# Kernel tuning notes

Hardware: AMD Instinct MI355X
Metric: run time of the kernel (lower is better)

## Reference

```python
import jax, jax.numpy as jnp
import numpy as np

B, N, D, L = 16, 100, 1024, 2000


def setup_inputs() -> dict:
    key = jax.random.key(0)
    ks = jax.random.split(key, 9)
    s = 1.0 / np.sqrt(D)
    return {
        "feature": jax.random.normal(ks[0], (B, N, D), dtype=jnp.float32),
        "graph": jax.random.randint(ks[1], (B, N, N), 0, L),
        "W0": jax.random.normal(ks[2], (D, D), dtype=jnp.float32) * s,
        "W1": jax.random.normal(ks[3], (D, D), dtype=jnp.float32) * s,
        "bias": jax.random.uniform(ks[4], (L, D), dtype=jnp.float32, minval=-s, maxval=s),
        "dp_Wa": jax.random.normal(ks[5], (D, D), dtype=jnp.float32) * s,
        "dp_ba": jax.random.normal(ks[6], (D,), dtype=jnp.float32) * s,
        "dp_Wb": jax.random.normal(ks[7], (D, D), dtype=jnp.float32) * s,
        "dp_bb": jax.random.normal(ks[8], (D,), dtype=jnp.float32) * s,
        "get_alpha": 0,
    }


def reference(feature, graph, W0, W1, bias, dp_Wa, dp_ba, dp_Wb, dp_bb, get_alpha):
    # ---- DirectedGraphConv.conv ----
    adj = (graph != 0).astype(feature.dtype)                     # [B,N,N]
    out = feature + feature @ W0.T + feature @ W1.T              # [B,N,D]
    out = out + jnp.take(bias, graph, axis=0).sum(axis=2)        # label-embedding gather+sum over neighbors
    # ---- relation_alpha: DotProduct(feature, feature) ----
    a = feature @ dp_Wa.T + dp_ba                                # [B,N,D]
    b = feature @ dp_Wb.T + dp_bb                                # [B,N,D]
    alpha = jnp.einsum('bik,bjk->bij', a, b)                     # [B,N,N]
    alpha = jnp.maximum(alpha, 0.0)                              # alpha[alpha<0]=0
    alpha = jnp.einsum('bij,bjk->bik', adj, alpha)               # bmm(adj, alpha)
    alpha = jax.nn.softmax(alpha, axis=1)                        # Softmax(dim=1)
    out = jnp.einsum('bij,bjk->bik', alpha, out)                 # bmm(alpha, output)
    if get_alpha:
        return (out, alpha)
    return out
```

## Files before the change

kernel.cpp:

```cpp
#include <hip/hip_runtime.h>
#include <stdint.h>

#define B_   16
#define N_   100
#define D_   1024
#define L_   2000
#define M_   1600

#define ZCAP 64
#define RCAP 24
#define TC   12

typedef __bf16 bf16x8 __attribute__((ext_vector_type(8)));
typedef float  f32x4  __attribute__((ext_vector_type(4)));

__device__ __forceinline__ void gl_lds16(const __bf16* g, __bf16* l) {
    __builtin_amdgcn_global_load_lds(
        (const __attribute__((address_space(1))) void*)g,
        (__attribute__((address_space(3))) void*)l, 16, 0, 0);
}


__global__ void __launch_bounds__(256)
k_prep(const float* __restrict__ f,
       const float* __restrict__ W0, const float* __restrict__ W1,
       const float* __restrict__ Wa, const float* __restrict__ Wb,
       const float* __restrict__ bias,
       __bf16* __restrict__ fb, __bf16* __restrict__ wcat, __bf16* __restrict__ biasB) {
    int i = blockIdx.x * 256 + threadIdx.x;
    union { __bf16 h[8]; uint4 u; } pk;
    if (i < 204800) {
        long base = (long)i * 8;
        const float4* p = (const float4*)(f + base);
        float4 x = p[0], y = p[1];
        pk.h[0]=(__bf16)x.x; pk.h[1]=(__bf16)x.y; pk.h[2]=(__bf16)x.z; pk.h[3]=(__bf16)x.w;
        pk.h[4]=(__bf16)y.x; pk.h[5]=(__bf16)y.y; pk.h[6]=(__bf16)y.z; pk.h[7]=(__bf16)y.w;
        ((uint4*)fb)[i] = pk.u;
    } else if (i < 598016) {
        int j = i - 204800;
        long base = (long)j * 8;
        long seg = base >> 20;
        long off = base & ((1l << 20) - 1);
        if (seg == 0) {
            const float4* p0 = (const float4*)(W0 + off);
            const float4* p1 = (const float4*)(W1 + off);
            float4 a0 = p0[0], a1 = p0[1], b0 = p1[0], b1 = p1[1];
            pk.h[0]=(__bf16)(a0.x+b0.x); pk.h[1]=(__bf16)(a0.y+b0.y);
            pk.h[2]=(__bf16)(a0.z+b0.z); pk.h[3]=(__bf16)(a0.w+b0.w);
            pk.h[4]=(__bf16)(a1.x+b1.x); pk.h[5]=(__bf16)(a1.y+b1.y);
            pk.h[6]=(__bf16)(a1.z+b1.z); pk.h[7]=(__bf16)(a1.w+b1.w);
        } else {
            const float* src = (seg == 1) ? Wa : Wb;
            const float4* p = (const float4*)(src + off);
            float4 x = p[0], y = p[1];
            pk.h[0]=(__bf16)x.x; pk.h[1]=(__bf16)x.y; pk.h[2]=(__bf16)x.z; pk.h[3]=(__bf16)x.w;
            pk.h[4]=(__bf16)y.x; pk.h[5]=(__bf16)y.y; pk.h[6]=(__bf16)y.z; pk.h[7]=(__bf16)y.w;
        }
        ((uint4*)wcat)[j] = pk.u;
    } else {
        int j = i - 598016;
        long base = (long)j * 8;
        const float4* p = (const float4*)(bias + base);
        float4 x = p[0], y = p[1];
        pk.h[0]=(__bf16)x.x; pk.h[1]=(__bf16)x.y; pk.h[2]=(__bf16)x.z; pk.h[3]=(__bf16)x.w;
        pk.h[4]=(__bf16)y.x; pk.h[5]=(__bf16)y.y; pk.h[6]=(__bf16)y.z; pk.h[7]=(__bf16)y.w;
        ((uint4*)biasB)[j] = pk.u;
    }
}


#define BM 64
#define BN 128
#define BK 64

__global__ void __launch_bounds__(256)
k_gemm(const __bf16* __restrict__ A, const __bf16* __restrict__ Bw,
       const float* __restrict__ feat, const float* __restrict__ ba,
       const float* __restrict__ bbias,
       float* __restrict__ out0, float* __restrict__ aB, float* __restrict__ bB) {
    __shared__ __align__(16) __bf16 As[BM * BK];
    __shared__ __align__(16) __bf16 Bs[BN * BK];
    int t = threadIdx.x;
    int bm = blockIdx.x, bn = blockIdx.y;
    int lane = t & 63, wave = t >> 6;
    int wr = wave & 1, wc = wave >> 1;
    int lrow = lane & 15, quad = lane >> 4;

    f32x4 acc[2][4] = {};
    const __bf16* Ag = A  + (long)(bm * BM) * D_;
    const __bf16* Bg = Bw + (long)(bn * BN) * D_;

    for (int k0 = 0; k0 < D_; k0 += BK) {
        #pragma unroll
        for (int pi = 0; pi < 2; ++pi) {
            int p = pi * 256 + t, row = p >> 3, c = (p & 7) ^ (row & 7);
            gl_lds16(Ag + (long)row * D_ + k0 + c * 8, As + p * 8);
        }
        #pragma unroll
        for (int pi = 0; pi < 4; ++pi) {
            int p = pi * 256 + t, row = p >> 3, c = (p & 7) ^ (row & 7);
            gl_lds16(Bg + (long)row * D_ + k0 + c * 8, Bs + p * 8);
        }
        __syncthreads();
        #pragma unroll
        for (int ks = 0; ks < 2; ++ks) {
            bf16x8 af[2], bf[4];
            #pragma unroll
            for (int i = 0; i < 2; ++i) {
                int r = wr * 32 + i * 16 + lrow;
                int slot = r * 8 + (((ks << 2) | quad) ^ (r & 7));
                af[i] = *(const bf16x8*)(As + slot * 8);
            }
            #pragma unroll
            for (int j = 0; j < 4; ++j) {
                int r = wc * 64 + j * 16 + lrow;
                int slot = r * 8 + (((ks << 2) | quad) ^ (r & 7));
                bf[j] = *(const bf16x8*)(Bs + slot * 8);
            }
            #pragma unroll
            for (int i = 0; i < 2; ++i)
                #pragma unroll
                for (int j = 0; j < 4; ++j)
                    acc[i][j] = __builtin_amdgcn_mfma_f32_16x16x32_bf16(af[i], bf[j], acc[i][j], 0, 0, 0);
        }
        __syncthreads();
    }

    int nbase = bn * BN;
    int seg = nbase >> 10;
    #pragma unroll
    for (int i = 0; i < 2; ++i) {
        int gm0 = bm * BM + wr * 32 + i * 16 + quad * 4;
        #pragma unroll
        for (int j = 0; j < 4; ++j) {
            int col = (nbase + wc * 64 + j * 16 + lrow) & 1023;
            #pragma unroll
            for (int r = 0; r < 4; ++r) {
                long m = gm0 + r;
                float v = acc[i][j][r];
                if (seg == 0)      out0[m * D_ + col] = v + feat[m * D_ + col];
                else if (seg == 1) aB[m * D_ + col]   = v + ba[col];
                else               bB[m * D_ + col]   = v + bbias[col];
            }
        }
    }
}


__global__ void __launch_bounds__(256)
k_gather(const int* __restrict__ graph, const __bf16* __restrict__ biasB,
         float* __restrict__ out0) {
    int bi = blockIdx.x;
    int t = threadIdx.x;
    __shared__ int idxs[N_];
    if (t < N_) idxs[t] = graph[(long)bi * N_ + t];
    __syncthreads();
    float a0 = 0.f, a1 = 0.f, a2 = 0.f, a3 = 0.f;
    for (int j = 0; j < N_; ++j) {
        int lb = idxs[j];
        union { uint2 u; __bf16 h[4]; } pk;
        pk.u = ((const uint2*)(biasB + (long)lb * D_))[t];
        a0 += (float)pk.h[0]; a1 += (float)pk.h[1];
        a2 += (float)pk.h[2]; a3 += (float)pk.h[3];
    }
    float4* o = (float4*)(out0 + (long)bi * D_) + t;
    float4 cur = *o;
    cur.x += a0; cur.y += a1; cur.z += a2; cur.w += a3;
    *o = cur;
}


__global__ void __launch_bounds__(256)
k_scan(const int* __restrict__ graph, int* __restrict__ meta) {
    int b = blockIdx.x, t = threadIdx.x;
    __shared__ int cnt, ndvS;
    __shared__ int zi[ZCAP], zj[ZCAP], pr[ZCAP], di[RCAP];
    if (t == 0) cnt = 0;
    __syncthreads();
    const int* g = graph + (long)b * N_ * N_;
    for (int p = t; p < N_ * N_; p += 256) {
        if (g[p] == 0) {
            int pos = atomicAdd(&cnt, 1);
            if (pos < ZCAP) { zi[pos] = p / N_; zj[pos] = p % N_; }
        }
    }
    __syncthreads();
    if (t == 0) {
        int Z = min(cnt, ZCAP), n = 0;
        for (int q = 0; q < Z; ++q) {
            int r = -1;
            for (int s = 0; s < n; ++s) if (di[s] == zi[q]) { r = s; break; }
            if (r < 0 && n < RCAP) { di[n] = zi[q]; r = n; ++n; }
            pr[q] = r;
        }
        ndvS = n;
    }
    __syncthreads();
    int Z = min(cnt, ZCAP), n = ndvS;
    int* mb = meta + b * 256;
    if (t == 0) { mb[0] = Z; mb[1] = n; }
    if (t < Z) { mb[2 + t] = zj[t]; mb[66 + t] = pr[t]; }
    if (t < n) mb[130 + t] = di[t];
    if (t < N_) {
        int m = 0;
        for (int r = 0; r < n; ++r) if (di[r] == t) m = 1 + r;
        mb[154 + t] = m;
    }
}


__global__ void __launch_bounds__(256)
k_alpha(const int* __restrict__ meta, const float* __restrict__ aB,
        const float* __restrict__ bB, float* __restrict__ wl, float* __restrict__ cwG) {
    int b = blockIdx.x, kc = blockIdx.y;
    int t = threadIdx.x, lane = t & 63, wave = t >> 6;
    const int* mb = meta + b * 256;
    int Z = mb[0], ndv = mb[1];
    __shared__ int zjL[ZCAP], prL[ZCAP];
    __shared__ float corrL[RCAP][4];
    __shared__ float wred[4][4];
    if (t < Z) { zjL[t] = mb[2 + t]; prL[t] = mb[66 + t]; }
    if (t < RCAP * 4) corrL[t >> 2][t & 3] = 0.f;
    __syncthreads();

    int k0 = kc * 4;
    float4 bv[4];
    #pragma unroll
    for (int kk = 0; kk < 4; ++kk)
        bv[kk] = *(const float4*)(bB + ((long)(b * N_ + k0 + kk)) * D_ + t * 4);

    for (int q = 0; q < Z; ++q) {
        const float* ar = aB + ((long)(b * N_ + zjL[q])) * D_;
        float4 av = *(const float4*)(ar + t * 4);
        float s[4];
        #pragma unroll
        for (int kk = 0; kk < 4; ++kk)
            s[kk] = av.x * bv[kk].x + av.y * bv[kk].y + av.z * bv[kk].z + av.w * bv[kk].w;
        #pragma unroll
        for (int off = 32; off > 0; off >>= 1)
            #pragma unroll
            for (int kk = 0; kk < 4; ++kk) s[kk] += __shfl_xor(s[kk], off);
        if (lane == 0) { wred[wave][0]=s[0]; wred[wave][1]=s[1]; wred[wave][2]=s[2]; wred[wave][3]=s[3]; }
        __syncthreads();
        if (t < 4) {
            float v = wred[0][t] + wred[1][t] + wred[2][t] + wred[3][t];
            v = fmaxf(v, 0.f);
            int r = prL[q];
            if (r >= 0) corrL[r][t] += v;
        }
        __syncthreads();
    }

    if (t < 4) {
        int k = k0 + t;
        float denom = (float)(N_ - ndv);
        for (int r = 0; r < ndv; ++r) {
            float e = __expf(-corrL[r][t]);
            corrL[r][t] = e;
            denom += e;
        }
        float w = 1.f / denom;
        wl[b * N_ + k] = w;
        for (int r = 0; r < ndv; ++r)
            cwG[((long)b * RCAP + r) * N_ + k] = corrL[r][t] * w;
    }
}


__global__ void __launch_bounds__(256)
k_mix(const int* __restrict__ meta, const float* __restrict__ wl,
      const float* __restrict__ cwG, const float* __restrict__ out0,
      float* __restrict__ out) {
    int b = blockIdx.x, dq = blockIdx.y;
    int t = threadIdx.x, c = t & 127, h = t >> 7;
    int d0 = dq * 128;
    const int* mb = meta + b * 256;
    int ndv = mb[1], ntask = ndv + 1;
    __shared__ float wT[TC][N_];
    __shared__ float parts[2][TC][128];
    __shared__ int mapL[N_];
    if (t < N_) mapL[t] = mb[154 + t];

    const float* o0 = out0 + (long)b * N_ * D_ + d0;
    for (int cb = 0; cb < ntask; cb += TC) {
        for (int idx = t; idx < TC * N_; idx += 256) {
            int rr = idx / N_, j = idx - rr * N_;
            int task = cb + rr;
            float v = 0.f;
            if (task == 0)         v = wl[b * N_ + j];
            else if (task <= ndv)  v = cwG[((long)b * RCAP + task - 1) * N_ + j];
            wT[rr][j] = v;
        }
        __syncthreads();
        float acc[TC] = {};
        #pragma unroll 2
        for (int j = h * 50; j < h * 50 + 50; ++j) {
            float v = o0[(long)j * D_ + c];
            #pragma unroll
            for (int rr = 0; rr < TC; ++rr) acc[rr] += wT[rr][j] * v;
        }
        #pragma unroll
        for (int rr = 0; rr < TC; ++rr) parts[h][rr][c] = acc[rr];
        __syncthreads();
        for (int i = h * 50; i < h * 50 + 50; ++i) {
            int task = mapL[i];
            if (task >= cb && task < cb + TC) {
                int rr = task - cb;
                out[((long)(b * N_ + i)) * D_ + d0 + c] = parts[0][rr][c] + parts[1][rr][c];
            }
        }
        __syncthreads();
    }
}


extern "C" void kernel_launch(void* const* d_in, const int* in_sizes, int n_in,
                              void* d_out, int out_size, void* d_ws, size_t ws_size,
                              hipStream_t stream) {
    const float* feature = (const float*)d_in[0];
    const int*   graph   = (const int*)d_in[1];
    const float* W0      = (const float*)d_in[2];
    const float* W1      = (const float*)d_in[3];
    const float* bias    = (const float*)d_in[4];
    const float* dp_Wa   = (const float*)d_in[5];
    const float* dp_ba   = (const float*)d_in[6];
    const float* dp_Wb   = (const float*)d_in[7];
    const float* dp_bb   = (const float*)d_in[8];
    float* out = (float*)d_out;

    char* w = (char*)d_ws;
    __bf16* fb16  = (__bf16*)(w);
    __bf16* wcat  = (__bf16*)(w + 3276800);
    __bf16* biasB = (__bf16*)(w + 9568256);
    float*  out0  = (float*)(w + 13664256);
    float*  aB    = (float*)(w + 20217856);
    float*  bB    = (float*)(w + 26771456);
    int*    meta  = (int*)(w + 33325056);
    float*  wl    = (float*)(w + 33341440);
    float*  cwG   = (float*)(w + 33347840);

    k_prep<<<3336, 256, 0, stream>>>(feature, W0, W1, dp_Wa, dp_Wb, bias,
                                     fb16, wcat, biasB);
    k_gemm<<<dim3(25, 24), 256, 0, stream>>>(fb16, wcat, feature, dp_ba, dp_bb,
                                             out0, aB, bB);
    k_gather<<<1600, 256, 0, stream>>>(graph, biasB, out0);
    k_scan<<<B_, 256, 0, stream>>>(graph, meta);
    k_alpha<<<dim3(B_, 25), 256, 0, stream>>>(meta, aB, bB, wl, cwG);
    k_mix<<<dim3(B_, 8), 256, 0, stream>>>(meta, wl, cwG, out0, out);
}
```

Measured before the change: 179.3 us.

## Double-buffer LDS tiles in projection GEMM to overlap loads with MFMA

```diff
diff --git a/kernel.cpp b/kernel.cpp
--- a/kernel.cpp
+++ b/kernel.cpp
@@ -78,8 +78,8 @@
        const float* __restrict__ feat, const float* __restrict__ ba,
        const float* __restrict__ bbias,
        float* __restrict__ out0, float* __restrict__ aB, float* __restrict__ bB) {
-    __shared__ __align__(16) __bf16 As[BM * BK];
-    __shared__ __align__(16) __bf16 Bs[BN * BK];
+    __shared__ __align__(16) __bf16 As[2][BM * BK];
+    __shared__ __align__(16) __bf16 Bs[2][BN * BK];
     int t = threadIdx.x;
     int bm = blockIdx.x, bn = blockIdx.y;
     int lane = t & 63, wave = t >> 6;
@@ -90,18 +90,35 @@
     const __bf16* Ag = A  + (long)(bm * BM) * D_;
     const __bf16* Bg = Bw + (long)(bn * BN) * D_;
 
-    for (int k0 = 0; k0 < D_; k0 += BK) {
+    {
         #pragma unroll
         for (int pi = 0; pi < 2; ++pi) {
             int p = pi * 256 + t, row = p >> 3, c = (p & 7) ^ (row & 7);
-            gl_lds16(Ag + (long)row * D_ + k0 + c * 8, As + p * 8);
+            gl_lds16(Ag + (long)row * D_ + c * 8, &As[0][p * 8]);
         }
         #pragma unroll
         for (int pi = 0; pi < 4; ++pi) {
             int p = pi * 256 + t, row = p >> 3, c = (p & 7) ^ (row & 7);
-            gl_lds16(Bg + (long)row * D_ + k0 + c * 8, Bs + p * 8);
-        }
-        __syncthreads();
+            gl_lds16(Bg + (long)row * D_ + c * 8, &Bs[0][p * 8]);
+        }
+    }
+
+    int stage = 0;
+    for (int k0 = 0; k0 < D_; k0 += BK) {
+        __syncthreads();
+        if (k0 + BK < D_) {
+            int kn = k0 + BK, so = stage ^ 1;
+            #pragma unroll
+            for (int pi = 0; pi < 2; ++pi) {
+                int p = pi * 256 + t, row = p >> 3, c = (p & 7) ^ (row & 7);
+                gl_lds16(Ag + (long)row * D_ + kn + c * 8, &As[so][p * 8]);
+            }
+            #pragma unroll
+            for (int pi = 0; pi < 4; ++pi) {
+                int p = pi * 256 + t, row = p >> 3, c = (p & 7) ^ (row & 7);
+                gl_lds16(Bg + (long)row * D_ + kn + c * 8, &Bs[so][p * 8]);
+            }
+        }
         #pragma unroll
         for (int ks = 0; ks < 2; ++ks) {
             bf16x8 af[2], bf[4];
@@ -109,13 +126,13 @@
             for (int i = 0; i < 2; ++i) {
                 int r = wr * 32 + i * 16 + lrow;
                 int slot = r * 8 + (((ks << 2) | quad) ^ (r & 7));
-                af[i] = *(const bf16x8*)(As + slot * 8);
+                af[i] = *(const bf16x8*)(&As[stage][slot * 8]);
             }
             #pragma unroll
             for (int j = 0; j < 4; ++j) {
                 int r = wc * 64 + j * 16 + lrow;
                 int slot = r * 8 + (((ks << 2) | quad) ^ (r & 7));
-                bf[j] = *(const bf16x8*)(Bs + slot * 8);
+                bf[j] = *(const bf16x8*)(&Bs[stage][slot * 8]);
             }
             #pragma unroll
             for (int i = 0; i < 2; ++i)
@@ -123,7 +140,7 @@
                 for (int j = 0; j < 4; ++j)
                     acc[i][j] = __builtin_amdgcn_mfma_f32_16x16x32_bf16(af[i], bf[j], acc[i][j], 0, 0, 0);
         }
-        __syncthreads();
+        stage ^= 1;
     }
 
     int nbase = bn * BN;
```

Result: slower. 184.4 us (+2.9%).
